# Kernel tuning notes

Measured on AMD Instinct MI355X. Metric: run time of the kernel, lower is better.

## Reference

```python
import jax, jax.numpy as jnp
import numpy as np

MASK_FILL = float(-2**32 + 1)


def setup_inputs() -> dict:
    key = jax.random.key(0)
    k1, k2, k3, k4, k5 = jax.random.split(key, 5)
    B, T, D = 64, 1024, 128
    return {
        "key": jax.random.normal(k1, (B, T, D), dtype=jnp.float32),
        "value": jax.random.normal(k2, (B, T, D), dtype=jnp.float32),
        "query": jax.random.normal(k3, (B, T, D), dtype=jnp.float32),
        "mask": jax.random.randint(k4, (B, T, T), 0, 2).astype(jnp.bool_),
        "query_mask": jax.random.uniform(k5, (B, T, 1), dtype=jnp.float32),
        "num_hidden": D,
    }


def reference(key, value, query, mask, query_mask, num_hidden):
    # scores: [B, Tq, Tk]
    scale = 1.0 / jnp.sqrt(jnp.float32(num_hidden))
    attn = jnp.einsum("bqd,bkd->bqk", query, key) * scale
    attn = jnp.where(mask, MASK_FILL, attn)
    attn = jax.nn.softmax(attn, axis=-1)
    attn = attn * query_mask  # broadcast [B, Tq, 1]
    result = jnp.einsum("bqk,bkd->bqd", attn, value)
    return (result, attn)
```

## Files before the change

kernel.cpp:

```cpp
#include <hip/hip_runtime.h>

#define B_   64
#define T_   1024
#define D_   128
#define SCALE_ 0.08838834764831845f
#define FILL_  (-4294967295.0f)

typedef __attribute__((ext_vector_type(8))) short short8v;
typedef __attribute__((ext_vector_type(4))) float f32x4;

#define MFMA16(A,Bv,C) __builtin_amdgcn_mfma_f32_16x16x32_bf16((A),(Bv),(C),0,0,0)

__device__ __forceinline__ void split8(const float f[8], short8v& h, short8v& l) {
#pragma unroll
    for (int i = 0; i < 8; ++i) {
        const unsigned int u = __float_as_uint(f[i]);
        h[i] = (short)(u >> 16);
        const float r = f[i] - __uint_as_float(u & 0xffff0000u);
        l[i] = (short)(__float_as_uint(r) >> 16);
    }
}
__device__ __forceinline__ unsigned int packsplit(float f) {
    const unsigned int u = __float_as_uint(f);
    const unsigned int hi = u >> 16;
    const float r = f - __uint_as_float(u & 0xffff0000u);
    const unsigned int lo = __float_as_uint(r) >> 16;
    return hi | (lo << 16);
}

__global__ __launch_bounds__(512, 4)
void mha_kernel(const float* __restrict__ Kp, const float* __restrict__ Vp,
                const float* __restrict__ Qp, const unsigned char* __restrict__ Mp,
                const float* __restrict__ QMp, float* __restrict__ Orp,
                float* __restrict__ Oap)
{
    __shared__ unsigned int Pc[128 * 33];
    __shared__ float redA[8 * 32];
    __shared__ float redB[8 * 32];

    const int tid  = threadIdx.x;
    const int w    = tid >> 6;
    const int lane = tid & 63;
    const int g    = lane >> 4;
    const int c    = lane & 15;
    const int wg   = (blockIdx.x & 7) * 256 + (blockIdx.x >> 3);
    const int b    = wg >> 5;
    const int q0   = (wg & 31) << 5;

    const unsigned int* mw = (const unsigned int*)Mp;
    unsigned int bad = 0u;
#pragma unroll
    for (int i = 0; i < 16; ++i) bad |= (unsigned int)(mw[i] > 1u);
    const bool m32 = (bad == 0u);

    const size_t bt = (size_t)b * T_;

    f32x4 acc[2][8];
#pragma unroll
    for (int mt = 0; mt < 2; ++mt)
#pragma unroll
        for (int nt = 0; nt < 8; ++nt) acc[mt][nt] = (f32x4)0.f;

#pragma unroll
    for (int ks = 0; ks < 4; ++ks) {
        short8v qh[2], ql[2];
#pragma unroll
        for (int mt = 0; mt < 2; ++mt) {
            const float* qp = Qp + (bt + q0 + mt*16 + c) * D_ + ks*32 + g*8;
            float f[8];
#pragma unroll
            for (int i = 0; i < 8; ++i) f[i] = qp[i];
            split8(f, qh[mt], ql[mt]);
        }
#pragma unroll
        for (int nt = 0; nt < 8; ++nt) {
            const float* kp = Kp + (bt + w*128 + nt*16 + c) * D_ + ks*32 + g*8;
            float f[8];
#pragma unroll
            for (int i = 0; i < 8; ++i) f[i] = kp[i];
            short8v kh, kl;
            split8(f, kh, kl);
#pragma unroll
            for (int mt = 0; mt < 2; ++mt) {
                acc[mt][nt] = MFMA16(qh[mt], kh, acc[mt][nt]);
                acc[mt][nt] = MFMA16(qh[mt], kl, acc[mt][nt]);
                acc[mt][nt] = MFMA16(ql[mt], kh, acc[mt][nt]);
            }
        }
    }

    float rmax[2][4];
#pragma unroll
    for (int mt = 0; mt < 2; ++mt)
#pragma unroll
    for (int rg = 0; rg < 4; ++rg) {
        const int row = mt*16 + g*4 + rg;
        const size_t mrow = (bt + q0 + row) * (size_t)T_ + w*128;
        float rm = -3.0e38f;
        if (m32) {
            const int* mi = (const int*)Mp;
#pragma unroll
            for (int nt = 0; nt < 8; ++nt) {
                float s = acc[mt][nt][rg] * SCALE_;
                if (mi[mrow + nt*16 + c]) s = FILL_;
                acc[mt][nt][rg] = s;
                rm = fmaxf(rm, s);
            }
        } else {
#pragma unroll
            for (int nt = 0; nt < 8; ++nt) {
                float s = acc[mt][nt][rg] * SCALE_;
                if (Mp[mrow + nt*16 + c]) s = FILL_;
                acc[mt][nt][rg] = s;
                rm = fmaxf(rm, s);
            }
        }
        rmax[mt][rg] = rm;
    }
#pragma unroll
    for (int mt = 0; mt < 2; ++mt)
#pragma unroll
    for (int rg = 0; rg < 4; ++rg)
#pragma unroll
        for (int off = 1; off < 16; off <<= 1)
            rmax[mt][rg] = fmaxf(rmax[mt][rg], __shfl_xor(rmax[mt][rg], off, 64));
    if (c == 0) {
#pragma unroll
        for (int mt = 0; mt < 2; ++mt)
#pragma unroll
        for (int rg = 0; rg < 4; ++rg)
            redA[w*32 + mt*16 + g*4 + rg] = rmax[mt][rg];
    }
    __syncthreads();
    float rsum[2][4];
#pragma unroll
    for (int mt = 0; mt < 2; ++mt)
#pragma unroll
    for (int rg = 0; rg < 4; ++rg) {
        const int row = mt*16 + g*4 + rg;
        float m = redA[row];
#pragma unroll
        for (int w2 = 1; w2 < 8; ++w2) m = fmaxf(m, redA[w2*32 + row]);
        float s = 0.f;
#pragma unroll
        for (int nt = 0; nt < 8; ++nt) {
            const float e = __expf(acc[mt][nt][rg] - m);
            acc[mt][nt][rg] = e;
            s += e;
        }
#pragma unroll
        for (int off = 1; off < 16; off <<= 1) s += __shfl_xor(s, off, 64);
        rsum[mt][rg] = s;
    }
    if (c == 0) {
#pragma unroll
        for (int mt = 0; mt < 2; ++mt)
#pragma unroll
        for (int rg = 0; rg < 4; ++rg)
            redB[w*32 + mt*16 + g*4 + rg] = rsum[mt][rg];
    }
    __syncthreads();

    unsigned int pk[2][8][4];
#pragma unroll
    for (int mt = 0; mt < 2; ++mt)
#pragma unroll
    for (int rg = 0; rg < 4; ++rg) {
        const int row = mt*16 + g*4 + rg;
        float ssum = redB[row];
#pragma unroll
        for (int w2 = 1; w2 < 8; ++w2) ssum += redB[w2*32 + row];
        const float inv = QMp[bt + q0 + row] / ssum;
        const size_t arow = (bt + q0 + row) * (size_t)T_ + w*128;
#pragma unroll
        for (int nt = 0; nt < 8; ++nt) {
            const float p = acc[mt][nt][rg] * inv;
            __builtin_nontemporal_store(p, &Oap[arow + nt*16 + c]);
            pk[mt][nt][rg] = packsplit(p);
        }
    }

    f32x4 o[2];
    o[0] = (f32x4)0.f;
    o[1] = (f32x4)0.f;

    for (int kc = 0; kc < 8; ++kc) {
        __syncthreads();
        if (w == kc) {
#pragma unroll
            for (int mt = 0; mt < 2; ++mt)
#pragma unroll
            for (int nt = 0; nt < 8; ++nt)
#pragma unroll
            for (int rg = 0; rg < 4; ++rg)
                Pc[(nt*16 + c)*33 + mt*16 + g*4 + rg] = pk[mt][nt][rg];
        }
        __syncthreads();
#pragma unroll
        for (int ks2 = 0; ks2 < 4; ++ks2) {
            short8v ph[2], pl[2];
#pragma unroll
            for (int mt = 0; mt < 2; ++mt) {
                const int base = (ks2*32 + g*8)*33 + mt*16 + c;
#pragma unroll
                for (int i = 0; i < 8; ++i) {
                    const unsigned int x = Pc[base + i*33];
                    ph[mt][i] = (short)(x & 0xffffu);
                    pl[mt][i] = (short)(x >> 16);
                }
            }
            float fv[8];
            {
                const float* vp = Vp + (bt + kc*128 + ks2*32 + g*8) * D_ + w*16 + c;
#pragma unroll
                for (int i = 0; i < 8; ++i) fv[i] = vp[(size_t)i * D_];
            }
            short8v vh, vl;
            split8(fv, vh, vl);
#pragma unroll
            for (int mt = 0; mt < 2; ++mt) {
                o[mt] = MFMA16(ph[mt], vh, o[mt]);
                o[mt] = MFMA16(ph[mt], vl, o[mt]);
                o[mt] = MFMA16(pl[mt], vh, o[mt]);
            }
        }
    }

#pragma unroll
    for (int mt = 0; mt < 2; ++mt)
#pragma unroll
    for (int rg = 0; rg < 4; ++rg)
        __builtin_nontemporal_store(o[mt][rg],
            &Orp[(bt + q0 + mt*16 + g*4 + rg) * D_ + w*16 + c]);
}

extern "C" void kernel_launch(void* const* d_in, const int* in_sizes, int n_in,
                              void* d_out, int out_size, void* d_ws, size_t ws_size,
                              hipStream_t stream)
{
    const float* Kp  = (const float*)d_in[0];
    const float* Vp  = (const float*)d_in[1];
    const float* Qp  = (const float*)d_in[2];
    const unsigned char* Mp = (const unsigned char*)d_in[3];
    const float* QMp = (const float*)d_in[4];
    float* Orp = (float*)d_out;
    float* Oap = Orp + (size_t)B_ * T_ * D_;

    hipLaunchKernelGGL(mha_kernel, dim3(B_ * 32), dim3(512), 0, stream,
                       Kp, Vp, Qp, Mp, QMp, Orp, Oap);
}
```

Before: 829.3 us.

## Stage attention probabilities through LDS for coalesced stores, reread from global for PV

Attention probabilities are now transposed through a per-wave LDS buffer so each row is written to the attention output with coalesced float4 stores, instead of scattered scalar nontemporal stores. The PV product no longer passes packed hi/lo probabilities between waves through shared memory with 16 block barriers. Each wave instead reloads the probabilities from the just-written global attention output, which relies on L2 hits and on visibility after a single __syncthreads. The result tile is also staged through LDS for coalesced float4 stores. The trade is more global reads and repeated hi/lo splitting against fewer barriers and better store coalescing.

```diff
diff --git a/kernel.cpp b/kernel.cpp
--- a/kernel.cpp
+++ b/kernel.cpp
@@ -19,13 +19,6 @@
         const float r = f[i] - __uint_as_float(u & 0xffff0000u);
         l[i] = (short)(__float_as_uint(r) >> 16);
     }
-}
-__device__ __forceinline__ unsigned int packsplit(float f) {
-    const unsigned int u = __float_as_uint(f);
-    const unsigned int hi = u >> 16;
-    const float r = f - __uint_as_float(u & 0xffff0000u);
-    const unsigned int lo = __float_as_uint(r) >> 16;
-    return hi | (lo << 16);
 }
 
 __global__ __launch_bounds__(512, 4)
@@ -34,7 +27,7 @@
                 const float* __restrict__ QMp, float* __restrict__ Orp,
                 float* __restrict__ Oap)
 {
-    __shared__ unsigned int Pc[128 * 33];
+    __shared__ __align__(16) float TBUF[8][8][132];
     __shared__ float redA[8 * 32];
     __shared__ float redB[8 * 32];
 
@@ -161,7 +154,6 @@
     }
     __syncthreads();
 
-    unsigned int pk[2][8][4];
 #pragma unroll
     for (int mt = 0; mt < 2; ++mt)
 #pragma unroll
@@ -171,67 +163,89 @@
 #pragma unroll
         for (int w2 = 1; w2 < 8; ++w2) ssum += redB[w2*32 + row];
         const float inv = QMp[bt + q0 + row] / ssum;
-        const size_t arow = (bt + q0 + row) * (size_t)T_ + w*128;
-#pragma unroll
-        for (int nt = 0; nt < 8; ++nt) {
-            const float p = acc[mt][nt][rg] * inv;
-            __builtin_nontemporal_store(p, &Oap[arow + nt*16 + c]);
-            pk[mt][nt][rg] = packsplit(p);
-        }
-    }
+#pragma unroll
+        for (int nt = 0; nt < 8; ++nt) acc[mt][nt][rg] *= inv;
+    }
+
+#pragma unroll
+    for (int r8 = 0; r8 < 4; ++r8) {
+        const int mt = r8 >> 1;
+        if ((g >> 1) == (r8 & 1)) {
+#pragma unroll
+            for (int nt = 0; nt < 8; ++nt)
+#pragma unroll
+            for (int rg = 0; rg < 4; ++rg)
+                TBUF[w][(g & 1) * 4 + rg][nt*16 + c] =
+                    (mt == 0) ? acc[0][nt][rg] : acc[1][nt][rg];
+        }
+        __asm__ __volatile__("s_waitcnt lgkmcnt(0)" ::: "memory");
+        __builtin_amdgcn_sched_barrier(0);
+#pragma unroll
+        for (int s = 0; s < 4; ++s) {
+            const int rl = 2*s + (lane >> 5);
+            const int q4 = (lane & 31) << 2;
+            float4 v;
+            v.x = TBUF[w][rl][q4 + 0];
+            v.y = TBUF[w][rl][q4 + 1];
+            v.z = TBUF[w][rl][q4 + 2];
+            v.w = TBUF[w][rl][q4 + 3];
+            *(float4*)&Oap[(bt + q0 + r8*8 + rl) * (size_t)T_ + w*128 + q4] = v;
+        }
+        __asm__ __volatile__("s_waitcnt lgkmcnt(0)" ::: "memory");
+        __builtin_amdgcn_sched_barrier(0);
+    }
+
+    __syncthreads();
 
     f32x4 o[2];
     o[0] = (f32x4)0.f;
     o[1] = (f32x4)0.f;
 
-    for (int kc = 0; kc < 8; ++kc) {
-        __syncthreads();
-        if (w == kc) {
-#pragma unroll
-            for (int mt = 0; mt < 2; ++mt)
-#pragma unroll
-            for (int nt = 0; nt < 8; ++nt)
-#pragma unroll
-            for (int rg = 0; rg < 4; ++rg)
-                Pc[(nt*16 + c)*33 + mt*16 + g*4 + rg] = pk[mt][nt][rg];
-        }
-        __syncthreads();
-#pragma unroll
-        for (int ks2 = 0; ks2 < 4; ++ks2) {
-            short8v ph[2], pl[2];
-#pragma unroll
-            for (int mt = 0; mt < 2; ++mt) {
-                const int base = (ks2*32 + g*8)*33 + mt*16 + c;
-#pragma unroll
-                for (int i = 0; i < 8; ++i) {
-                    const unsigned int x = Pc[base + i*33];
-                    ph[mt][i] = (short)(x & 0xffffu);
-                    pl[mt][i] = (short)(x >> 16);
-                }
-            }
-            float fv[8];
-            {
-                const float* vp = Vp + (bt + kc*128 + ks2*32 + g*8) * D_ + w*16 + c;
-#pragma unroll
-                for (int i = 0; i < 8; ++i) fv[i] = vp[(size_t)i * D_];
-            }
-            short8v vh, vl;
-            split8(fv, vh, vl);
-#pragma unroll
-            for (int mt = 0; mt < 2; ++mt) {
-                o[mt] = MFMA16(ph[mt], vh, o[mt]);
-                o[mt] = MFMA16(ph[mt], vl, o[mt]);
-                o[mt] = MFMA16(pl[mt], vh, o[mt]);
-            }
-        }
-    }
-
+    for (int ch = 0; ch < 32; ++ch) {
+        short8v ph[2], pl[2];
+#pragma unroll
+        for (int mt = 0; mt < 2; ++mt) {
+            const float* pp = Oap + (bt + q0 + mt*16 + c) * (size_t)T_ + ch*32 + g*8;
+            float f[8];
+#pragma unroll
+            for (int i = 0; i < 8; ++i) f[i] = pp[i];
+            split8(f, ph[mt], pl[mt]);
+        }
+        float fv[8];
+        {
+            const float* vp = Vp + (bt + ch*32 + g*8) * D_ + w*16 + c;
+#pragma unroll
+            for (int i = 0; i < 8; ++i) fv[i] = vp[(size_t)i * D_];
+        }
+        short8v vh, vl;
+        split8(fv, vh, vl);
+#pragma unroll
+        for (int mt = 0; mt < 2; ++mt) {
+            o[mt] = MFMA16(ph[mt], vh, o[mt]);
+            o[mt] = MFMA16(ph[mt], vl, o[mt]);
+            o[mt] = MFMA16(pl[mt], vh, o[mt]);
+        }
+    }
+
+    float (*RB)[132] = (float (*)[132])&TBUF[0][0][0];
 #pragma unroll
     for (int mt = 0; mt < 2; ++mt)
 #pragma unroll
     for (int rg = 0; rg < 4; ++rg)
-        __builtin_nontemporal_store(o[mt][rg],
-            &Orp[(bt + q0 + mt*16 + g*4 + rg) * D_ + w*16 + c]);
+        RB[mt*16 + g*4 + rg][w*16 + c] = o[mt][rg];
+    __syncthreads();
+#pragma unroll
+    for (int it = 0; it < 2; ++it) {
+        const int idx = it*512 + tid;
+        const int row = idx >> 5;
+        const int q4  = (idx & 31) << 2;
+        float4 v;
+        v.x = RB[row][q4 + 0];
+        v.y = RB[row][q4 + 1];
+        v.z = RB[row][q4 + 2];
+        v.w = RB[row][q4 + 3];
+        *(float4*)&Orp[(bt + q0 + row) * D_ + q4] = v;
+    }
 }
 
 extern "C" void kernel_launch(void* const* d_in, const int* in_sizes, int n_in,
```

Result: slower. 857.8 us (+3.4%).
